# Kernel optimization log

Hardware: AMD Instinct MI355X
Metric: run time of the kernel (lower is better)

Reference implementation:

```python
import jax, jax.numpy as jnp
import numpy as np

C = 8           # feat_channel
B, N = 8, 64    # batch, max objects
H, W = 128, 128
D = (C + 2) * C + C + C * C + C + C + 1  # 169


def setup_inputs() -> dict:
    key = jax.random.key(0)
    k1, k2, k3, k4 = jax.random.split(key, 4)
    seg_feat = jax.random.normal(k1, (B, C, H, W), dtype=jnp.float32)
    conv_weight = jax.random.normal(k2, (B, D, H, W), dtype=jnp.float32)
    mask = jnp.ones((B, N), dtype=jnp.float32)
    ind = jax.random.randint(k3, (B, N), 0, H * W, dtype=jnp.int64)
    target = jax.random.uniform(k4, (B, N, H, W), dtype=jnp.float32)
    return {"seg_feat": seg_feat, "conv_weight": conv_weight, "mask": mask,
            "ind": ind, "target": target}


def reference(seg_feat, conv_weight, mask, ind, target):
    b, c, h, w = seg_feat.shape
    n = ind.shape[1]
    # _tranpose_and_gather_feat: [B,D,H,W] -> [B,HW,D] -> gather at ind -> [B,N,D]
    wflat = conv_weight.reshape(b, -1, h * w).transpose(0, 2, 1)
    weight = jnp.take_along_axis(wflat, ind[:, :, None], axis=1)  # [B,N,D]
    splits = np.cumsum([(c + 2) * c, c, c * c, c, c])
    w1, b1, w2, b2, w3, b3 = jnp.split(weight, splits, axis=-1)
    w1 = w1.reshape(b, n, c, c + 2)   # per-object conv1 1x1 weights
    w2 = w2.reshape(b, n, c, c)
    w3 = w3.reshape(b, n, 1, c)
    # object centers and relative coordinate maps
    x0 = (ind % w).astype(jnp.float32)
    y0 = (ind // w).astype(jnp.float32)
    xg = jnp.arange(w, dtype=jnp.float32)
    yg = jnp.arange(h, dtype=jnp.float32)
    y_grid, x_grid = jnp.meshgrid(yg, xg, indexing="ij")  # [H,W]
    x_rel = (x_grid[None, None] - x0[:, :, None, None]) / 128.0  # [B,N,H,W]
    y_rel = (y_grid[None, None] - y0[:, :, None, None]) / 128.0
    feat = jnp.concatenate(
        [jnp.broadcast_to(seg_feat[:, None], (b, n, c, h, w)),
         x_rel[:, :, None], y_rel[:, :, None]], axis=2)  # [B,N,C+2,H,W]
    # three grouped 1x1 convs == per-object channel contractions
    h1 = jax.nn.relu(jnp.einsum("bnoc,bnchw->bnohw", w1, feat) + b1[..., None, None])
    h2 = jax.nn.relu(jnp.einsum("bnoc,bnchw->bnohw", w2, h1) + b2[..., None, None])
    out = jax.nn.sigmoid(jnp.einsum("bnoc,bnchw->bnohw", w3, h2) + b3[..., None, None])[:, :, 0]  # [B,N,H,W]
    m = mask[:, :, None, None]
    pred = out * m
    tgt = target * m
    smooth = 1.0
    inter = jnp.sum(pred * tgt, axis=(1, 2, 3))
    denom = jnp.sum(pred * pred, axis=(1, 2, 3)) + jnp.sum(tgt * tgt, axis=(1, 2, 3))
    loss = 1.0 - (2.0 * inter + smooth) / (denom + smooth)  # per-image dice
    return jnp.mean(loss)  # sum over batch / batch_size
```

## Files before the change

### kernel.cpp

```cpp
#include <hip/hip_runtime.h>

#define Cc 8
#define Hh 128
#define Ww 128
#define Nn 64
#define Bb 8
#define Dd 169
#define HW (Hh * Ww)
#define CHUNKS 4
#define NBLK (Bb * Nn * CHUNKS)
#define PXB (HW / CHUNKS)
#define GROUPS 4
#define WSTRIDE 88
#define RED_OFF (Bb * Nn * WSTRIDE)

#define INV128 (1.0f / 128.0f)

typedef __fp16 f16x2 __attribute__((ext_vector_type(2)));

static __device__ __forceinline__ f16x2 pk(float a, float b) {
    return __builtin_amdgcn_cvt_pkrtz(a, b);
}
static __device__ __forceinline__ uint32_t pku(float a, float b) {
    f16x2 t = pk(a, b); uint32_t u; __builtin_memcpy(&u, &t, 4); return u;
}
static __device__ __forceinline__ f16x2 u2h(uint32_t u) {
    f16x2 r; __builtin_memcpy(&r, &u, 4); return r;
}
static __device__ __forceinline__ f16x2 max2(f16x2 a, f16x2 b) {
    return __builtin_elementwise_max(a, b);
}

static __device__ __forceinline__ void fma_lo(f16x2& acc, uint32_t w, f16x2 f) {
    asm("v_pk_fma_f16 %0, %1, %2, %0 op_sel:[0,0,0] op_sel_hi:[0,1,1]"
        : "+v"(acc) : "s"(w), "v"(f));
}
static __device__ __forceinline__ void fma_hi(f16x2& acc, uint32_t w, f16x2 f) {
    asm("v_pk_fma_f16 %0, %1, %2, %0 op_sel:[1,0,0] op_sel_hi:[1,1,1]"
        : "+v"(acc) : "s"(w), "v"(f));
}
static __device__ __forceinline__ f16x2 fma_lo4(uint32_t w, f16x2 f, f16x2 c) {
    f16x2 o;
    asm("v_pk_fma_f16 %0, %1, %2, %3 op_sel:[0,0,0] op_sel_hi:[0,1,1]"
        : "=v"(o) : "s"(w), "v"(f), "v"(c));
    return o;
}
static __device__ __forceinline__ f16x2 fma_hi4(uint32_t w, f16x2 f, f16x2 c) {
    f16x2 o;
    asm("v_pk_fma_f16 %0, %1, %2, %3 op_sel:[1,0,0] op_sel_hi:[1,1,1]"
        : "=v"(o) : "s"(w), "v"(f), "v"(c));
    return o;
}

static __device__ __forceinline__ float pick(float4 v, int j) {
    return j == 0 ? v.x : j == 1 ? v.y : j == 2 ? v.z : v.w;
}

__global__ void pack_weights(const float* __restrict__ conv_weight,
                             const int*   __restrict__ ind,
                             uint32_t*    __restrict__ wt) {
    const int bn = blockIdx.x;
    const int j  = threadIdx.x;
    const int b  = bn >> 6;
    const int ind_bn = ind[bn];
    const float* src = conv_weight + (size_t)b * Dd * HW + ind_bn;
    if (j < 85) {
        int d0, d1;
        if (j < 40)      { d0 = (j / 5) * 10 + (j % 5) * 2; d1 = d0 + 1; }
        else if (j < 72) { d0 = 88  + 2 * (j - 40); d1 = d0 + 1; }
        else if (j < 76) { d0 = 160 + 2 * (j - 72); d1 = d0 + 1; }
        else if (j < 80) { d0 = 80  + 2 * (j - 76); d1 = d0 + 1; }
        else if (j < 84) { d0 = 152 + 2 * (j - 80); d1 = d0 + 1; }
        else             { d0 = 168; d1 = -1; }
        const float a = src[(size_t)d0 * HW];
        const float c = (d1 >= 0) ? src[(size_t)d1 * HW] : 0.f;
        wt[bn * WSTRIDE + j] = pku(a, c);
    }
}

__global__ __launch_bounds__(256)
void seg_dice_main(const float* __restrict__ seg_feat,
                   const float* __restrict__ mask,
                   const int*   __restrict__ ind,
                   const float* __restrict__ target,
                   const uint32_t* __restrict__ wtab,
                   float* __restrict__ red_base) {
    const int g     = (blockIdx.x & 7) * (NBLK / 8) + (blockIdx.x >> 3);
    const int chunk = g & (CHUNKS - 1);
    const int bnu = __builtin_amdgcn_readfirstlane(g >> 2);
    const int b   = bnu >> 6;
    const int tid = threadIdx.x;

    uint32_t wq[88];
    {
        const uint4* wt4 = (const uint4*)(wtab + bnu * WSTRIDE);
        #pragma unroll
        for (int k = 0; k < 22; ++k) {
            const uint4 q = wt4[k];
            wq[4 * k + 0] = q.x; wq[4 * k + 1] = q.y;
            wq[4 * k + 2] = q.z; wq[4 * k + 3] = q.w;
        }
    }
    f16x2 b1v[8], b2v[8];
    #pragma unroll
    for (int k = 0; k < 4; ++k) {
        const f16x2 p1 = u2h(wq[76 + k]);
        b1v[2 * k]     = f16x2{p1.x, p1.x};
        b1v[2 * k + 1] = f16x2{p1.y, p1.y};
        const f16x2 p2 = u2h(wq[80 + k]);
        b2v[2 * k]     = f16x2{p2.x, p2.x};
        b2v[2 * k + 1] = f16x2{p2.y, p2.y};
    }
    const f16x2 pb3 = u2h(wq[84]);
    const f16x2 b3v = f16x2{pb3.x, pb3.x};

    const int   ind_bn = ind[bnu];
    const float m  = mask[bnu];
    const float x0 = (float)(ind_bn & (Ww - 1));
    const float y0 = (float)(ind_bn >> 7);

    const float* seg_b  = seg_feat + (size_t)b * Cc * HW;
    const float* tgt_bn = target   + (size_t)bnu * HW;

    float inter = 0.f, ps = 0.f, ts = 0.f;
    const int pbase = chunk * PXB + (tid << 2);

    #pragma unroll 1
    for (int it = 0; it < GROUPS; ++it) {
        const int p = pbase + (it << 10);

        const float4 t4 = *(const float4*)(tgt_bn + p);
        float4 f4[8];
        #pragma unroll
        for (int c = 0; c < 8; ++c) f4[c] = *(const float4*)(seg_b + c * HW + p);

        const float yrf = ((float)(p >> 7)        - y0) * INV128;
        const float xbf = ((float)(p & (Ww - 1)) - x0) * INV128;
        const f16x2 yr2  = pk(yrf, yrf);
        const f16x2 xr01 = pk(xbf, xbf + INV128);
        const f16x2 xr23 = pk(xbf + 2.f * INV128, xbf + 3.f * INV128);

        f16x2 fA[8], fB[8];
        #pragma unroll
        for (int c = 0; c < 8; ++c) {
            fA[c] = pk(f4[c].x, f4[c].y);
            fB[c] = pk(f4[c].z, f4[c].w);
        }

        f16x2 h1A[8], h1B[8];
        #pragma unroll
        for (int o = 0; o < 8; ++o) {
            const uint32_t wxy = wq[5 * o + 4];
            const f16x2 base = fma_hi4(wxy, yr2, b1v[o]);
            f16x2 a01 = fma_lo4(wxy, xr01, base);
            f16x2 a23 = fma_lo4(wxy, xr23, base);
            #pragma unroll
            for (int k = 0; k < 4; ++k) {
                const uint32_t w = wq[5 * o + k];
                fma_lo(a01, w, fA[2 * k]);  fma_hi(a01, w, fA[2 * k + 1]);
                fma_lo(a23, w, fB[2 * k]);  fma_hi(a23, w, fB[2 * k + 1]);
            }
            const f16x2 z = {(__fp16)0.f, (__fp16)0.f};
            h1A[o] = max2(a01, z);
            h1B[o] = max2(a23, z);
        }

        f16x2 h2A[8], h2B[8];
        #pragma unroll
        for (int o = 0; o < 8; ++o) {
            const uint32_t w0 = wq[40 + 4 * o];
            f16x2 a01 = fma_lo4(w0, h1A[0], b2v[o]);
            f16x2 a23 = fma_lo4(w0, h1B[0], b2v[o]);
            fma_hi(a01, w0, h1A[1]);  fma_hi(a23, w0, h1B[1]);
            #pragma unroll
            for (int k = 1; k < 4; ++k) {
                const uint32_t w = wq[40 + 4 * o + k];
                fma_lo(a01, w, h1A[2 * k]);  fma_hi(a01, w, h1A[2 * k + 1]);
                fma_lo(a23, w, h1B[2 * k]);  fma_hi(a23, w, h1B[2 * k + 1]);
            }
            const f16x2 z = {(__fp16)0.f, (__fp16)0.f};
            h2A[o] = max2(a01, z);
            h2B[o] = max2(a23, z);
        }

        f16x2 z01 = fma_lo4(wq[72], h2A[0], b3v);
        f16x2 z23 = fma_lo4(wq[72], h2B[0], b3v);
        fma_hi(z01, wq[72], h2A[1]);  fma_hi(z23, wq[72], h2B[1]);
        #pragma unroll
        for (int k = 1; k < 4; ++k) {
            const uint32_t w = wq[72 + k];
            fma_lo(z01, w, h2A[2 * k]);  fma_hi(z01, w, h2A[2 * k + 1]);
            fma_lo(z23, w, h2B[2 * k]);  fma_hi(z23, w, h2B[2 * k + 1]);
        }

        const float o0 = __builtin_amdgcn_rcpf(1.f + __expf(-(float)z01.x));
        const float o1 = __builtin_amdgcn_rcpf(1.f + __expf(-(float)z01.y));
        const float o2 = __builtin_amdgcn_rcpf(1.f + __expf(-(float)z23.x));
        const float o3 = __builtin_amdgcn_rcpf(1.f + __expf(-(float)z23.y));

        inter = fmaf(o0, t4.x, inter); inter = fmaf(o1, t4.y, inter);
        inter = fmaf(o2, t4.z, inter); inter = fmaf(o3, t4.w, inter);
        ps = fmaf(o0, o0, ps); ps = fmaf(o1, o1, ps);
        ps = fmaf(o2, o2, ps); ps = fmaf(o3, o3, ps);
        ts = fmaf(t4.x, t4.x, ts); ts = fmaf(t4.y, t4.y, ts);
        ts = fmaf(t4.z, t4.z, ts); ts = fmaf(t4.w, t4.w, ts);
    }

    const float m2 = m * m;
    inter *= m2; ps *= m2; ts *= m2;

    #pragma unroll
    for (int off = 32; off > 0; off >>= 1) {
        inter += __shfl_down(inter, off);
        ps    += __shfl_down(ps,    off);
        ts    += __shfl_down(ts,    off);
    }
    __shared__ float red[3][4];
    const int wave = tid >> 6;
    if ((tid & 63) == 0) { red[0][wave] = inter; red[1][wave] = ps; red[2][wave] = ts; }
    __syncthreads();
    if (tid == 0) {
        const int local = (bnu & 63) * CHUNKS + chunk;
        red_base[(b * 3 + 0) * 256 + local] = red[0][0] + red[0][1] + red[0][2] + red[0][3];
        red_base[(b * 3 + 1) * 256 + local] = red[1][0] + red[1][1] + red[1][2] + red[1][3];
        red_base[(b * 3 + 2) * 256 + local] = red[2][0] + red[2][1] + red[2][2] + red[2][3];
    }
}

__global__ void seg_dice_final(const float* __restrict__ red_base, float* __restrict__ out) {
    __shared__ float red[24][4];
    const int tid = threadIdx.x;
    if (tid < 96) {
        const int series = tid >> 2;
        const int part   = tid & 3;
        const float4* p = (const float4*)(red_base + series * 256 + part * 64);
        float s = 0.f;
        #pragma unroll
        for (int i = 0; i < 16; ++i) { const float4 v = p[i]; s += (v.x + v.y) + (v.z + v.w); }
        red[series][part] = s;
    }
    __syncthreads();
    if (tid == 0) {
        float acc = 0.f;
        #pragma unroll
        for (int b = 0; b < Bb; ++b) {
            const float inter = red[b*3+0][0] + red[b*3+0][1] + red[b*3+0][2] + red[b*3+0][3];
            const float p2    = red[b*3+1][0] + red[b*3+1][1] + red[b*3+1][2] + red[b*3+1][3];
            const float t2    = red[b*3+2][0] + red[b*3+2][1] + red[b*3+2][2] + red[b*3+2][3];
            acc += 1.0f - (2.0f * inter + 1.0f) / (p2 + t2 + 1.0f);
        }
        out[0] = acc * (1.0f / (float)Bb);
    }
}

extern "C" void kernel_launch(void* const* d_in, const int* in_sizes, int n_in,
                              void* d_out, int out_size, void* d_ws, size_t ws_size,
                              hipStream_t stream) {
    const float* seg_feat    = (const float*)d_in[0];
    const float* conv_weight = (const float*)d_in[1];
    const float* mask        = (const float*)d_in[2];
    const int*   ind         = (const int*)d_in[3];
    const float* target      = (const float*)d_in[4];
    float* out = (float*)d_out;
    float* ws  = (float*)d_ws;

    uint32_t* wtab     = (uint32_t*)ws;
    float*    red_base = ws + RED_OFF;

    pack_weights<<<Bb * Nn, 96, 0, stream>>>(conv_weight, ind, wtab);
    seg_dice_main<<<NBLK, 256, 0, stream>>>(seg_feat, mask, ind, target, wtab, red_base);
    seg_dice_final<<<1, 128, 0, stream>>>(red_base, out);
}
```

Before: 41.55 us.

## Reuse seg_feat pixels across groups of objects per block

Each block now covers one pixel slice for a group of 8 objects, not 4 pixel groups for a single object. The seg_feat loads and their fp16 conversion happen once per block and are reused across the 8 objects, which cuts seg_feat traffic per object. The cost is reloading the 88-word weight table, mask and index on every object iteration, and the block ordering changes from object-major to batch-interleaved. The partial-sum slot count drops from 256 to 128 per series, so the final reduction reads fewer values.

```diff
diff --git a/kernel.cpp b/kernel.cpp
--- a/kernel.cpp
+++ b/kernel.cpp
@@ -7,12 +7,14 @@
 #define Bb 8
 #define Dd 169
 #define HW (Hh * Ww)
-#define CHUNKS 4
-#define NBLK (Bb * Nn * CHUNKS)
+#define GN 8
+#define NGRP (Nn / GN)
+#define CHUNKS 16
+#define NBLK (Bb * NGRP * CHUNKS)
 #define PXB (HW / CHUNKS)
-#define GROUPS 4
 #define WSTRIDE 88
 #define RED_OFF (Bb * Nn * WSTRIDE)
+#define SLOTS (NGRP * CHUNKS)
 
 #define INV128 (1.0f / 128.0f)
 
@@ -50,10 +52,6 @@
     asm("v_pk_fma_f16 %0, %1, %2, %3 op_sel:[1,0,0] op_sel_hi:[1,1,1]"
         : "=v"(o) : "s"(w), "v"(f), "v"(c));
     return o;
-}
-
-static __device__ __forceinline__ float pick(float4 v, int j) {
-    return j == 0 ? v.x : j == 1 ? v.y : j == 2 ? v.z : v.w;
 }
 
 __global__ void pack_weights(const float* __restrict__ conv_weight,
@@ -85,67 +83,72 @@
                    const float* __restrict__ target,
                    const uint32_t* __restrict__ wtab,
                    float* __restrict__ red_base) {
-    const int g     = (blockIdx.x & 7) * (NBLK / 8) + (blockIdx.x >> 3);
-    const int chunk = g & (CHUNKS - 1);
-    const int bnu = __builtin_amdgcn_readfirstlane(g >> 2);
-    const int b   = bnu >> 6;
-    const int tid = threadIdx.x;
-
-    uint32_t wq[88];
-    {
-        const uint4* wt4 = (const uint4*)(wtab + bnu * WSTRIDE);
-        #pragma unroll
-        for (int k = 0; k < 22; ++k) {
-            const uint4 q = wt4[k];
-            wq[4 * k + 0] = q.x; wq[4 * k + 1] = q.y;
-            wq[4 * k + 2] = q.z; wq[4 * k + 3] = q.w;
-        }
-    }
-    f16x2 b1v[8], b2v[8];
+    const int bid   = blockIdx.x;
+    const int b     = bid & 7;
+    const int t     = bid >> 3;
+    const int ngrp  = t >> 4;
+    const int chunk = t & (CHUNKS - 1);
+    const int tid   = threadIdx.x;
+
+    const int p = chunk * PXB + (tid << 2);
+
+    const float* seg_b = seg_feat + (size_t)b * Cc * HW;
+    f16x2 sA[8], sB[8];
     #pragma unroll
-    for (int k = 0; k < 4; ++k) {
-        const f16x2 p1 = u2h(wq[76 + k]);
-        b1v[2 * k]     = f16x2{p1.x, p1.x};
-        b1v[2 * k + 1] = f16x2{p1.y, p1.y};
-        const f16x2 p2 = u2h(wq[80 + k]);
-        b2v[2 * k]     = f16x2{p2.x, p2.x};
-        b2v[2 * k + 1] = f16x2{p2.y, p2.y};
-    }
-    const f16x2 pb3 = u2h(wq[84]);
-    const f16x2 b3v = f16x2{pb3.x, pb3.x};
-
-    const int   ind_bn = ind[bnu];
-    const float m  = mask[bnu];
-    const float x0 = (float)(ind_bn & (Ww - 1));
-    const float y0 = (float)(ind_bn >> 7);
-
-    const float* seg_b  = seg_feat + (size_t)b * Cc * HW;
-    const float* tgt_bn = target   + (size_t)bnu * HW;
+    for (int c = 0; c < 8; ++c) {
+        const float4 v = *(const float4*)(seg_b + c * HW + p);
+        sA[c] = pk(v.x, v.y);
+        sB[c] = pk(v.z, v.w);
+    }
+    const float xf = (float)(p & (Ww - 1)) * INV128;
+    const float yf = (float)(p >> 7) * INV128;
+    const f16x2 xq01 = pk(xf, xf + INV128);
+    const f16x2 xq23 = pk(xf + 2.f * INV128, xf + 3.f * INV128);
+    const f16x2 yq   = pk(yf, yf);
+
+    const int bnb = __builtin_amdgcn_readfirstlane(b * Nn + ngrp * GN);
 
     float inter = 0.f, ps = 0.f, ts = 0.f;
-    const int pbase = chunk * PXB + (tid << 2);
 
     #pragma unroll 1
-    for (int it = 0; it < GROUPS; ++it) {
-        const int p = pbase + (it << 10);
-
-        const float4 t4 = *(const float4*)(tgt_bn + p);
-        float4 f4[8];
-        #pragma unroll
-        for (int c = 0; c < 8; ++c) f4[c] = *(const float4*)(seg_b + c * HW + p);
-
-        const float yrf = ((float)(p >> 7)        - y0) * INV128;
-        const float xbf = ((float)(p & (Ww - 1)) - x0) * INV128;
-        const f16x2 yr2  = pk(yrf, yrf);
-        const f16x2 xr01 = pk(xbf, xbf + INV128);
-        const f16x2 xr23 = pk(xbf + 2.f * INV128, xbf + 3.f * INV128);
-
-        f16x2 fA[8], fB[8];
-        #pragma unroll
-        for (int c = 0; c < 8; ++c) {
-            fA[c] = pk(f4[c].x, f4[c].y);
-            fB[c] = pk(f4[c].z, f4[c].w);
-        }
+    for (int n = 0; n < GN; ++n) {
+        const int bn = bnb + n;
+
+        const float4 t4 = *(const float4*)(target + (size_t)bn * HW + p);
+
+        uint32_t wq[88];
+        {
+            const uint4* wt4 = (const uint4*)(wtab + bn * WSTRIDE);
+            #pragma unroll
+            for (int k = 0; k < 22; ++k) {
+                const uint4 q = wt4[k];
+                wq[4 * k + 0] = q.x; wq[4 * k + 1] = q.y;
+                wq[4 * k + 2] = q.z; wq[4 * k + 3] = q.w;
+            }
+        }
+        const float m  = mask[bn];
+        const int   ib = ind[bn];
+
+        const float x0 = (float)(ib & (Ww - 1)) * INV128;
+        const float y0 = (float)(ib >> 7) * INV128;
+        const f16x2 x0s = pk(x0, x0);
+        const f16x2 y0s = pk(y0, y0);
+        const f16x2 xr01 = xq01 - x0s;
+        const f16x2 xr23 = xq23 - x0s;
+        const f16x2 yr2  = yq   - y0s;
+
+        f16x2 b1v[8], b2v[8];
+        #pragma unroll
+        for (int k = 0; k < 4; ++k) {
+            const f16x2 p1 = u2h(wq[76 + k]);
+            b1v[2 * k]     = f16x2{p1.x, p1.x};
+            b1v[2 * k + 1] = f16x2{p1.y, p1.y};
+            const f16x2 p2 = u2h(wq[80 + k]);
+            b2v[2 * k]     = f16x2{p2.x, p2.x};
+            b2v[2 * k + 1] = f16x2{p2.y, p2.y};
+        }
+        const f16x2 pb3 = u2h(wq[84]);
+        const f16x2 b3v = f16x2{pb3.x, pb3.x};
 
         f16x2 h1A[8], h1B[8];
         #pragma unroll
@@ -157,8 +160,8 @@
             #pragma unroll
             for (int k = 0; k < 4; ++k) {
                 const uint32_t w = wq[5 * o + k];
-                fma_lo(a01, w, fA[2 * k]);  fma_hi(a01, w, fA[2 * k + 1]);
-                fma_lo(a23, w, fB[2 * k]);  fma_hi(a23, w, fB[2 * k + 1]);
+                fma_lo(a01, w, sA[2 * k]);  fma_hi(a01, w, sA[2 * k + 1]);
+                fma_lo(a23, w, sB[2 * k]);  fma_hi(a23, w, sB[2 * k + 1]);
             }
             const f16x2 z = {(__fp16)0.f, (__fp16)0.f};
             h1A[o] = max2(a01, z);
@@ -198,16 +201,19 @@
         const float o2 = __builtin_amdgcn_rcpf(1.f + __expf(-(float)z23.x));
         const float o3 = __builtin_amdgcn_rcpf(1.f + __expf(-(float)z23.y));
 
-        inter = fmaf(o0, t4.x, inter); inter = fmaf(o1, t4.y, inter);
-        inter = fmaf(o2, t4.z, inter); inter = fmaf(o3, t4.w, inter);
-        ps = fmaf(o0, o0, ps); ps = fmaf(o1, o1, ps);
-        ps = fmaf(o2, o2, ps); ps = fmaf(o3, o3, ps);
-        ts = fmaf(t4.x, t4.x, ts); ts = fmaf(t4.y, t4.y, ts);
-        ts = fmaf(t4.z, t4.z, ts); ts = fmaf(t4.w, t4.w, ts);
-    }
-
-    const float m2 = m * m;
-    inter *= m2; ps *= m2; ts *= m2;
+        float in_ = 0.f, ps_ = 0.f, ts_ = 0.f;
+        in_ = fmaf(o0, t4.x, in_); in_ = fmaf(o1, t4.y, in_);
+        in_ = fmaf(o2, t4.z, in_); in_ = fmaf(o3, t4.w, in_);
+        ps_ = fmaf(o0, o0, ps_); ps_ = fmaf(o1, o1, ps_);
+        ps_ = fmaf(o2, o2, ps_); ps_ = fmaf(o3, o3, ps_);
+        ts_ = fmaf(t4.x, t4.x, ts_); ts_ = fmaf(t4.y, t4.y, ts_);
+        ts_ = fmaf(t4.z, t4.z, ts_); ts_ = fmaf(t4.w, t4.w, ts_);
+
+        const float m2 = m * m;
+        inter = fmaf(m2, in_, inter);
+        ps    = fmaf(m2, ps_, ps);
+        ts    = fmaf(m2, ts_, ts);
+    }
 
     #pragma unroll
     for (int off = 32; off > 0; off >>= 1) {
@@ -220,10 +226,9 @@
     if ((tid & 63) == 0) { red[0][wave] = inter; red[1][wave] = ps; red[2][wave] = ts; }
     __syncthreads();
     if (tid == 0) {
-        const int local = (bnu & 63) * CHUNKS + chunk;
-        red_base[(b * 3 + 0) * 256 + local] = red[0][0] + red[0][1] + red[0][2] + red[0][3];
-        red_base[(b * 3 + 1) * 256 + local] = red[1][0] + red[1][1] + red[1][2] + red[1][3];
-        red_base[(b * 3 + 2) * 256 + local] = red[2][0] + red[2][1] + red[2][2] + red[2][3];
+        red_base[(b * 3 + 0) * SLOTS + t] = red[0][0] + red[0][1] + red[0][2] + red[0][3];
+        red_base[(b * 3 + 1) * SLOTS + t] = red[1][0] + red[1][1] + red[1][2] + red[1][3];
+        red_base[(b * 3 + 2) * SLOTS + t] = red[2][0] + red[2][1] + red[2][2] + red[2][3];
     }
 }
 
@@ -233,10 +238,10 @@
     if (tid < 96) {
         const int series = tid >> 2;
         const int part   = tid & 3;
-        const float4* p = (const float4*)(red_base + series * 256 + part * 64);
+        const float4* p = (const float4*)(red_base + series * SLOTS + part * 32);
         float s = 0.f;
         #pragma unroll
-        for (int i = 0; i < 16; ++i) { const float4 v = p[i]; s += (v.x + v.y) + (v.z + v.w); }
+        for (int i = 0; i < 8; ++i) { const float4 v = p[i]; s += (v.x + v.y) + (v.z + v.w); }
         red[series][part] = s;
     }
     __syncthreads();
```

New measurement: 42.43 us. +2.1%, slower.
